# Performance work log

Hardware: AMD Instinct MI355X
Metric: run time of the kernel (lower is better)

## Reference

```python
import jax, jax.numpy as jnp
import numpy as np
from jax import lax

FPLANE = 256
RATIO = 0.5
C_SHIFT = int(FPLANE * RATIO)  # 128
HALF = C_SHIFT // 2            # 64


def setup_inputs() -> dict:
    key = jax.random.key(0)
    k_x, k_wl, k_bl, k_wr, k_br = jax.random.split(key, 5)
    T, C, H, W = 64, FPLANE, 56, 56
    x = jax.random.normal(k_x, (T, C, H, W), dtype=jnp.float32)
    # Conv3d(HALF -> 1, kernel (3,3,3)); original inits to zero, we use small
    # random weights so the gated path is non-trivial for kernel testing.
    scale = 1.0 / np.sqrt(HALF * 27)
    w_l = jax.random.normal(k_wl, (1, HALF, 3, 3, 3), dtype=jnp.float32) * scale
    b_l = jax.random.normal(k_bl, (1,), dtype=jnp.float32) * 0.01
    w_r = jax.random.normal(k_wr, (1, HALF, 3, 3, 3), dtype=jnp.float32) * scale
    b_r = jax.random.normal(k_br, (1,), dtype=jnp.float32) * 0.01
    return {"x": x, "w_l": w_l, "b_l": b_l, "w_r": w_r, "b_r": b_r}


def _cyclic_pad_t(x):
    # x: (1, C, T, H, W) -> pad 1 frame cyclically along T
    return jnp.concatenate([x[:, :, -1:], x, x[:, :, :1]], axis=2)


def _conv3d(x, w, b):
    # temporal padding VALID (input is cyclically pre-padded), spatial SAME
    y = lax.conv_general_dilated(
        x, w, window_strides=(1, 1, 1),
        padding=[(0, 0), (1, 1), (1, 1)],
        dimension_numbers=("NCDHW", "OIDHW", "NCDHW"))
    return y + b[None, :, None, None, None]


def reference(x, w_l, b_l, w_r, b_r):
    # x: (T, C, H, W) -> (1, C, T, H, W)
    x5 = x.transpose(1, 0, 2, 3)[None]
    x_l = x5[:, :HALF]                 # (1, half, T, H, W)
    x_r = x5[:, HALF:C_SHIFT]
    x_keep = x5[:, C_SHIFT:]

    gate_l = jnp.tanh(_conv3d(_cyclic_pad_t(x_l), w_l, b_l))  # (1,1,T,H,W)
    gate_r = jnp.tanh(_conv3d(_cyclic_pad_t(x_r), w_r, b_r))

    y_l = gate_l * x_l
    y_r = gate_r * x_r
    y_l = jnp.roll(y_l, -1, axis=2) + (x_l - y_l)
    y_r = jnp.roll(y_r, 1, axis=2) + (x_r - y_r)

    y_all = jnp.concatenate([y_l, y_r, x_keep], axis=1)  # (1, C, T, H, W)
    return y_all[0].transpose(1, 0, 2, 3)                # (T, C, H, W)
```

## Files before the change

kernel.cpp:

```cpp
#include <hip/hip_runtime.h>
#include <math.h>

#define T_DIM 64
#define C_DIM 256
#define H_DIM 56
#define W_DIM 56
#define HW    (H_DIM * W_DIM)
#define HW4   (HW / 4)
#define CHW   (C_DIM * HW)
#define THW   (T_DIM * HW)

typedef float nt_float4 __attribute__((ext_vector_type(4)));

__device__ __forceinline__ float rfl(float v) {
    return __int_as_float(__builtin_amdgcn_readfirstlane(__float_as_int(v)));
}

__global__ __launch_bounds__(256) void gate_copy_kernel(
    const float* __restrict__ x,
    const float* __restrict__ w_l,
    const float* __restrict__ b_l,
    const float* __restrict__ w_r,
    const float* __restrict__ b_r,
    float* __restrict__ gbuf,
    float* __restrict__ out)
{
    constexpr int NGATE = 256;
    const int p = blockIdx.x;

    if (p >= NGATE) {
        const int qq     = p - NGATE;
        const int tchunk = qq / 392;
        const int bx2    = qq - tchunk * 392;
        const int tid    = 128 * HW4 + bx2 * 256 + (int)threadIdx.x;
        const int t0     = tchunk * 16;

        const nt_float4* xn4 = (const nt_float4*)x;
        nt_float4*       on4 = (nt_float4*)out;
        const size_t ts = C_DIM * HW4;

        #pragma unroll 4
        for (int i = 0; i < 16; ++i) {
            const size_t idx = (size_t)(t0 + i) * ts + tid;
            nt_float4 v = __builtin_nontemporal_load(&xn4[idx]);
            __builtin_nontemporal_store(v, &on4[idx]);
        }
        return;
    }

    __shared__ float4 red[4][7][64];

    const int xcd  = p & 7;
    const int r    = p >> 3;
    const int tl   = r & 7;
    const int side = (r >> 3) & 1;
    const int hh   = (r >> 4) & 1;
    const int t    = xcd * 8 + tl;

    const int waveid = __builtin_amdgcn_readfirstlane((int)(threadIdx.x >> 6));
    const int lane = threadIdx.x & 63;
    const int wg   = lane & 15;
    const int rg   = lane >> 4;
    const bool act = (wg < 14);
    const int w0   = act ? wg * 4 : 52;
    const int r0   = hh * 28 + rg * 7;
    const bool have_l = (wg > 0);
    const bool have_r = (wg < 13);

    const float* wtab = (side ? w_r : w_l) + waveid * 16 * 27;
    const int c0 = side * 64 + waveid * 16;

    const int tm = (t + 63) & 63, tp = (t + 1) & 63;
    const float* tbase[3] = { x + (size_t)tm * CHW,
                              x + (size_t)t  * CHW,
                              x + (size_t)tp * CHW };

    float acc[7][4];
    #pragma unroll
    for (int j = 0; j < 7; ++j)
        #pragma unroll
        for (int k = 0; k < 4; ++k) acc[j][k] = 0.f;

    #pragma unroll 1
    for (int ci = 0; ci < 16; ++ci) {
        float wgt[27];
        #pragma unroll
        for (int k = 0; k < 27; ++k) wgt[k] = rfl(wtab[ci * 27 + k]);

        #pragma unroll
        for (int dt = 0; dt < 3; ++dt) {
            const float* plane = tbase[dt] + (size_t)(c0 + ci) * HW;

            #pragma unroll
            for (int s9 = 0; s9 < 9; ++s9) {
                const int sr = r0 - 1 + s9;
                bool rv = true;
                int  srow = sr;
                if (s9 == 0)      { rv = (sr >= 0);     srow = rv ? sr : 0; }
                else if (s9 == 8) { rv = (sr < H_DIM);  srow = rv ? sr : (H_DIM - 1); }

                const float* row = plane + srow * W_DIM;
                float4 m  = *(const float4*)(row + w0);
                float  fl = __shfl_up(m.w, 1);
                float  fr = __shfl_down(m.x, 1);

                float f0 = have_l ? fl : 0.f;
                float f1 = m.x, f2 = m.y, f3 = m.z, f4v = m.w;
                float f5 = have_r ? fr : 0.f;
                if ((s9 == 0 || s9 == 8) && !rv) {
                    f0 = 0.f; f1 = 0.f; f2 = 0.f; f3 = 0.f; f4v = 0.f; f5 = 0.f;
                }
                float f[6] = { f0, f1, f2, f3, f4v, f5 };

                const int jlo = (s9 >= 2) ? s9 - 2 : 0;
                const int jhi = (s9 <= 6) ? s9 : 6;
                #pragma unroll
                for (int j = jlo; j <= jhi; ++j) {
                    const int dh = s9 - j;
                    const float w0t = wgt[dt * 9 + dh * 3 + 0];
                    const float w1t = wgt[dt * 9 + dh * 3 + 1];
                    const float w2t = wgt[dt * 9 + dh * 3 + 2];
                    #pragma unroll
                    for (int k = 0; k < 4; ++k)
                        acc[j][k] += w0t * f[k] + w1t * f[k + 1] + w2t * f[k + 2];
                }
            }
        }
    }

    #pragma unroll
    for (int j = 0; j < 7; ++j) {
        float4 v; v.x = acc[j][0]; v.y = acc[j][1]; v.z = acc[j][2]; v.w = acc[j][3];
        red[waveid][j][lane] = v;
    }
    __syncthreads();

    if (waveid == 0 && act) {
        const float bias = side ? b_r[0] : b_l[0];
        float* pp = gbuf + (size_t)side * THW
                         + (size_t)t * HW + r0 * W_DIM + w0;
        #pragma unroll
        for (int j = 0; j < 7; ++j) {
            float4 a = red[0][j][lane], b2 = red[1][j][lane];
            float4 c = red[2][j][lane], d  = red[3][j][lane];
            float4 v;
            v.x = tanhf((a.x + b2.x) + (c.x + d.x) + bias);
            v.y = tanhf((a.y + b2.y) + (c.y + d.y) + bias);
            v.z = tanhf((a.z + b2.z) + (c.z + d.z) + bias);
            v.w = tanhf((a.w + b2.w) + (c.w + d.w) + bias);
            *(float4*)(pp + j * W_DIM) = v;
        }
    }
}

__global__ __launch_bounds__(256) void combine_kernel(
    const float* __restrict__ x,
    const float* __restrict__ g,
    float* __restrict__ out)
{
    const int tid = blockIdx.x * 256 + threadIdx.x;
    const int t0  = blockIdx.y * 16;
    const int c   = tid / HW4;
    const int gb  = tid - c * HW4;

    const float4* x4 = (const float4*)x;
    nt_float4*    on4 = (nt_float4*)out;
    const size_t  ts = C_DIM * HW4;
    const size_t  base = tid;

    if (c < 64) {
        const float4* gl4 = (const float4*)g;
        float4 xv = x4[(size_t)t0 * ts + base];
        float4 g0 = gl4[t0 * HW4 + gb];
        #pragma unroll 4
        for (int i = 0; i < 16; ++i) {
            const int t  = t0 + i;
            const int tp = (t + 1) & 63;
            float4 xn = x4[(size_t)tp * ts + base];
            float4 g1 = gl4[tp * HW4 + gb];
            nt_float4 r;
            r.x = xv.x - g0.x * xv.x + g1.x * xn.x;
            r.y = xv.y - g0.y * xv.y + g1.y * xn.y;
            r.z = xv.z - g0.z * xv.z + g1.z * xn.z;
            r.w = xv.w - g0.w * xv.w + g1.w * xn.w;
            __builtin_nontemporal_store(r, &on4[(size_t)t * ts + base]);
            xv = xn; g0 = g1;
        }
    } else {
        const float4* gr4 = (const float4*)(g + THW);
        const int tmi = (t0 + 63) & 63;
        float4 xm = x4[(size_t)tmi * ts + base];
        float4 gm = gr4[tmi * HW4 + gb];
        #pragma unroll 4
        for (int i = 0; i < 16; ++i) {
            const int t = t0 + i;
            float4 xv = x4[(size_t)t * ts + base];
            float4 g0 = gr4[t * HW4 + gb];
            nt_float4 r;
            r.x = xv.x - g0.x * xv.x + gm.x * xm.x;
            r.y = xv.y - g0.y * xv.y + gm.y * xm.y;
            r.z = xv.z - g0.z * xv.z + gm.z * xm.z;
            r.w = xv.w - g0.w * xv.w + gm.w * xm.w;
            __builtin_nontemporal_store(r, &on4[(size_t)t * ts + base]);
            xm = xv; gm = g0;
        }
    }
}

extern "C" void kernel_launch(void* const* d_in, const int* in_sizes, int n_in,
                              void* d_out, int out_size, void* d_ws, size_t ws_size,
                              hipStream_t stream) {
    const float* x   = (const float*)d_in[0];
    const float* w_l = (const float*)d_in[1];
    const float* b_l = (const float*)d_in[2];
    const float* w_r = (const float*)d_in[3];
    const float* b_r = (const float*)d_in[4];
    float* out  = (float*)d_out;
    float* gbuf = (float*)d_ws;

    const int ngate = 256;
    const int ncopy = 392 * 4;
    gate_copy_kernel<<<ngate + ncopy, 256, 0, stream>>>(x, w_l, b_l, w_r, b_r,
                                                        gbuf, out);
    combine_kernel<<<dim3(392, 4), 256, 0, stream>>>(x, gbuf, out);
}
```

Before: 125.9 us.

## Split gate conv channels across 16 waves with tree reduction in LDS

Raises the gate/copy kernel block size from 256 to 1024 threads, so each gate block uses 16 waves, each handling 4 input channels instead of 16. Per-wave partial sums are combined with a log-step tree reduction through shared memory. The copy blocks are resized to match the new block size. The aim is to shorten the serial channel loop and spread the gate work over more waves, at the cost of extra barriers, more reduction traffic, and possible register pressure under 1024-thread launch bounds.

```diff
diff --git a/kernel.cpp b/kernel.cpp
--- a/kernel.cpp
+++ b/kernel.cpp
@@ -16,7 +16,7 @@
     return __int_as_float(__builtin_amdgcn_readfirstlane(__float_as_int(v)));
 }
 
-__global__ __launch_bounds__(256) void gate_copy_kernel(
+__global__ __launch_bounds__(1024) void gate_copy_kernel(
     const float* __restrict__ x,
     const float* __restrict__ w_l,
     const float* __restrict__ b_l,
@@ -26,13 +26,15 @@
     float* __restrict__ out)
 {
     constexpr int NGATE = 256;
+    __shared__ float4 red[8][7][64];
+
     const int p = blockIdx.x;
 
     if (p >= NGATE) {
         const int qq     = p - NGATE;
-        const int tchunk = qq / 392;
-        const int bx2    = qq - tchunk * 392;
-        const int tid    = 128 * HW4 + bx2 * 256 + (int)threadIdx.x;
+        const int tchunk = qq / 98;
+        const int bx2    = qq - tchunk * 98;
+        const int tid    = 128 * HW4 + bx2 * 1024 + (int)threadIdx.x;
         const int t0     = tchunk * 16;
 
         const nt_float4* xn4 = (const nt_float4*)x;
@@ -47,8 +49,6 @@
         }
         return;
     }
-
-    __shared__ float4 red[4][7][64];
 
     const int xcd  = p & 7;
     const int r    = p >> 3;
@@ -67,8 +67,8 @@
     const bool have_l = (wg > 0);
     const bool have_r = (wg < 13);
 
-    const float* wtab = (side ? w_r : w_l) + waveid * 16 * 27;
-    const int c0 = side * 64 + waveid * 16;
+    const float* wtab = (side ? w_r : w_l) + waveid * 4 * 27;
+    const int c0 = side * 64 + waveid * 4;
 
     const int tm = (t + 63) & 63, tp = (t + 1) & 63;
     const float* tbase[3] = { x + (size_t)tm * CHW,
@@ -82,7 +82,7 @@
         for (int k = 0; k < 4; ++k) acc[j][k] = 0.f;
 
     #pragma unroll 1
-    for (int ci = 0; ci < 16; ++ci) {
+    for (int ci = 0; ci < 4; ++ci) {
         float wgt[27];
         #pragma unroll
         for (int k = 0; k < 27; ++k) wgt[k] = rfl(wtab[ci * 27 + k]);
@@ -129,11 +129,26 @@
     }
 
     #pragma unroll
-    for (int j = 0; j < 7; ++j) {
-        float4 v; v.x = acc[j][0]; v.y = acc[j][1]; v.z = acc[j][2]; v.w = acc[j][3];
-        red[waveid][j][lane] = v;
-    }
-    __syncthreads();
+    for (int n = 8; n >= 1; n >>= 1) {
+        if (waveid >= n && waveid < 2 * n) {
+            #pragma unroll
+            for (int j = 0; j < 7; ++j) {
+                float4 v; v.x = acc[j][0]; v.y = acc[j][1];
+                          v.z = acc[j][2]; v.w = acc[j][3];
+                red[waveid - n][j][lane] = v;
+            }
+        }
+        __syncthreads();
+        if (waveid < n) {
+            #pragma unroll
+            for (int j = 0; j < 7; ++j) {
+                float4 v = red[waveid][j][lane];
+                acc[j][0] += v.x; acc[j][1] += v.y;
+                acc[j][2] += v.z; acc[j][3] += v.w;
+            }
+        }
+        if (n > 1) __syncthreads();
+    }
 
     if (waveid == 0 && act) {
         const float bias = side ? b_r[0] : b_l[0];
@@ -141,13 +156,11 @@
                          + (size_t)t * HW + r0 * W_DIM + w0;
         #pragma unroll
         for (int j = 0; j < 7; ++j) {
-            float4 a = red[0][j][lane], b2 = red[1][j][lane];
-            float4 c = red[2][j][lane], d  = red[3][j][lane];
             float4 v;
-            v.x = tanhf((a.x + b2.x) + (c.x + d.x) + bias);
-            v.y = tanhf((a.y + b2.y) + (c.y + d.y) + bias);
-            v.z = tanhf((a.z + b2.z) + (c.z + d.z) + bias);
-            v.w = tanhf((a.w + b2.w) + (c.w + d.w) + bias);
+            v.x = tanhf(acc[j][0] + bias);
+            v.y = tanhf(acc[j][1] + bias);
+            v.z = tanhf(acc[j][2] + bias);
+            v.w = tanhf(acc[j][3] + bias);
             *(float4*)(pp + j * W_DIM) = v;
         }
     }
@@ -219,8 +232,8 @@
     float* gbuf = (float*)d_ws;
 
     const int ngate = 256;
-    const int ncopy = 392 * 4;
-    gate_copy_kernel<<<ngate + ncopy, 256, 0, stream>>>(x, w_l, b_l, w_r, b_r,
-                                                        gbuf, out);
+    const int ncopy = 392;
+    gate_copy_kernel<<<ngate + ncopy, 1024, 0, stream>>>(x, w_l, b_l, w_r, b_r,
+                                                         gbuf, out);
     combine_kernel<<<dim3(392, 4), 256, 0, stream>>>(x, gbuf, out);
 }
```

Result: slower. 289.7 us (+130.1%).

## Split gate conv channel reduction across four blocks with atomic last-block finalize

Applied to the files above, without the earlier changes.

Splits each gate tile's 64-channel reduction into four blocks of 16 channels, raising the gate grid from 256 to 1024 blocks. Each block writes partial sums to a workspace buffer, and an atomic counter picks the last-arriving block to sum the four partials, apply bias and tanh, and write the gate. This targets the long per-block serial conv loop and poor GPU fill from only 256 gate blocks. In exchange it adds partial-sum global traffic, a memset launch, and fence/atomic synchronisation.

```diff
diff --git a/kernel.cpp b/kernel.cpp
--- a/kernel.cpp
+++ b/kernel.cpp
@@ -9,6 +9,10 @@
 #define HW4   (HW / 4)
 #define CHW   (C_DIM * HW)
 #define THW   (T_DIM * HW)
+#define PL4   (THW / 4)
+#define TS4   (C_DIM * HW4)
+#define NGATE 1024
+#define NCOPY 1568
 
 typedef float nt_float4 __attribute__((ext_vector_type(4)));
 
@@ -22,26 +26,27 @@
     const float* __restrict__ b_l,
     const float* __restrict__ w_r,
     const float* __restrict__ b_r,
+    float* __restrict__ pbuf,
     float* __restrict__ gbuf,
-    float* __restrict__ out)
+    float* __restrict__ out,
+    unsigned int* __restrict__ cnt)
 {
-    constexpr int NGATE = 256;
-    const int p = blockIdx.x;
+    const int p   = blockIdx.x;
+    const int tid = threadIdx.x;
 
     if (p >= NGATE) {
         const int qq     = p - NGATE;
         const int tchunk = qq / 392;
         const int bx2    = qq - tchunk * 392;
-        const int tid    = 128 * HW4 + bx2 * 256 + (int)threadIdx.x;
+        const int col    = 128 * HW4 + bx2 * 256 + tid;
         const int t0     = tchunk * 16;
 
         const nt_float4* xn4 = (const nt_float4*)x;
         nt_float4*       on4 = (nt_float4*)out;
-        const size_t ts = C_DIM * HW4;
 
         #pragma unroll 4
         for (int i = 0; i < 16; ++i) {
-            const size_t idx = (size_t)(t0 + i) * ts + tid;
+            const size_t idx = (size_t)(t0 + i) * TS4 + col;
             nt_float4 v = __builtin_nontemporal_load(&xn4[idx]);
             __builtin_nontemporal_store(v, &on4[idx]);
         }
@@ -49,16 +54,19 @@
     }
 
     __shared__ float4 red[4][7][64];
-
-    const int xcd  = p & 7;
-    const int r    = p >> 3;
-    const int tl   = r & 7;
-    const int side = (r >> 3) & 1;
-    const int hh   = (r >> 4) & 1;
-    const int t    = xcd * 8 + tl;
-
-    const int waveid = __builtin_amdgcn_readfirstlane((int)(threadIdx.x >> 6));
-    const int lane = threadIdx.x & 63;
+    __shared__ int    lastflag;
+
+    const int xcd   = p & 7;
+    const int j     = p >> 3;
+    const int gq    = j & 3;
+    const int tileL = j >> 2;
+    const int tl    = tileL & 7;
+    const int side  = (tileL >> 3) & 1;
+    const int hh    = tileL >> 4;
+    const int t     = xcd * 8 + tl;
+
+    const int waveid = __builtin_amdgcn_readfirstlane(tid >> 6);
+    const int lane = tid & 63;
     const int wg   = lane & 15;
     const int rg   = lane >> 4;
     const bool act = (wg < 14);
@@ -67,8 +75,9 @@
     const bool have_l = (wg > 0);
     const bool have_r = (wg < 13);
 
-    const float* wtab = (side ? w_r : w_l) + waveid * 16 * 27;
-    const int c0 = side * 64 + waveid * 16;
+    const int cw = gq * 16 + waveid * 4;
+    const float* wtab = (side ? w_r : w_l) + cw * 27;
+    const int c0 = side * 64 + cw;
 
     const int tm = (t + 63) & 63, tp = (t + 1) & 63;
     const float* tbase[3] = { x + (size_t)tm * CHW,
@@ -77,12 +86,12 @@
 
     float acc[7][4];
     #pragma unroll
-    for (int j = 0; j < 7; ++j)
+    for (int jj = 0; jj < 7; ++jj)
         #pragma unroll
-        for (int k = 0; k < 4; ++k) acc[j][k] = 0.f;
+        for (int k = 0; k < 4; ++k) acc[jj][k] = 0.f;
 
     #pragma unroll 1
-    for (int ci = 0; ci < 16; ++ci) {
+    for (int ci = 0; ci < 4; ++ci) {
         float wgt[27];
         #pragma unroll
         for (int k = 0; k < 27; ++k) wgt[k] = rfl(wtab[ci * 27 + k]);
@@ -115,40 +124,70 @@
                 const int jlo = (s9 >= 2) ? s9 - 2 : 0;
                 const int jhi = (s9 <= 6) ? s9 : 6;
                 #pragma unroll
-                for (int j = jlo; j <= jhi; ++j) {
-                    const int dh = s9 - j;
+                for (int jj = jlo; jj <= jhi; ++jj) {
+                    const int dh = s9 - jj;
                     const float w0t = wgt[dt * 9 + dh * 3 + 0];
                     const float w1t = wgt[dt * 9 + dh * 3 + 1];
                     const float w2t = wgt[dt * 9 + dh * 3 + 2];
                     #pragma unroll
                     for (int k = 0; k < 4; ++k)
-                        acc[j][k] += w0t * f[k] + w1t * f[k + 1] + w2t * f[k + 2];
+                        acc[jj][k] += w0t * f[k] + w1t * f[k + 1] + w2t * f[k + 2];
                 }
             }
         }
     }
 
     #pragma unroll
-    for (int j = 0; j < 7; ++j) {
-        float4 v; v.x = acc[j][0]; v.y = acc[j][1]; v.z = acc[j][2]; v.w = acc[j][3];
-        red[waveid][j][lane] = v;
+    for (int jj = 0; jj < 7; ++jj) {
+        float4 v; v.x = acc[jj][0]; v.y = acc[jj][1];
+                  v.z = acc[jj][2]; v.w = acc[jj][3];
+        red[waveid][jj][lane] = v;
     }
     __syncthreads();
 
-    if (waveid == 0 && act) {
+    const int sg = side * 4 + gq;
+    if (waveid == 0) {
+        if (act) {
+            float* pp = pbuf + (size_t)sg * THW
+                             + (size_t)t * HW + r0 * W_DIM + w0;
+            #pragma unroll
+            for (int jj = 0; jj < 7; ++jj) {
+                float4 a = red[0][jj][lane], b2 = red[1][jj][lane];
+                float4 c = red[2][jj][lane], d  = red[3][jj][lane];
+                float4 v;
+                v.x = (a.x + b2.x) + (c.x + d.x);
+                v.y = (a.y + b2.y) + (c.y + d.y);
+                v.z = (a.z + b2.z) + (c.z + d.z);
+                v.w = (a.w + b2.w) + (c.w + d.w);
+                *(float4*)(pp + jj * W_DIM) = v;
+            }
+        }
+        __threadfence();
+        if (tid == 0) {
+            unsigned old = atomicAdd(&cnt[xcd * 32 + tileL], 1u);
+            lastflag = (old == 3u);
+        }
+    }
+    __syncthreads();
+
+    if (lastflag) {
+        __threadfence();
         const float bias = side ? b_r[0] : b_l[0];
-        float* pp = gbuf + (size_t)side * THW
-                         + (size_t)t * HW + r0 * W_DIM + w0;
-        #pragma unroll
-        for (int j = 0; j < 7; ++j) {
-            float4 a = red[0][j][lane], b2 = red[1][j][lane];
-            float4 c = red[2][j][lane], d  = red[3][j][lane];
+        const float4* p4 = (const float4*)pbuf;
+        float4* g4 = (float4*)gbuf;
+        const int base4 = t * HW4 + hh * 392;
+
+        for (int i = tid; i < 392; i += 256) {
+            float4 a = p4[(size_t)(side * 4 + 0) * PL4 + base4 + i];
+            float4 b = p4[(size_t)(side * 4 + 1) * PL4 + base4 + i];
+            float4 c = p4[(size_t)(side * 4 + 2) * PL4 + base4 + i];
+            float4 d = p4[(size_t)(side * 4 + 3) * PL4 + base4 + i];
             float4 v;
-            v.x = tanhf((a.x + b2.x) + (c.x + d.x) + bias);
-            v.y = tanhf((a.y + b2.y) + (c.y + d.y) + bias);
-            v.z = tanhf((a.z + b2.z) + (c.z + d.z) + bias);
-            v.w = tanhf((a.w + b2.w) + (c.w + d.w) + bias);
-            *(float4*)(pp + j * W_DIM) = v;
+            v.x = tanhf((a.x + b.x) + (c.x + d.x) + bias);
+            v.y = tanhf((a.y + b.y) + (c.y + d.y) + bias);
+            v.z = tanhf((a.z + b.z) + (c.z + d.z) + bias);
+            v.w = tanhf((a.w + b.w) + (c.w + d.w) + bias);
+            g4[(size_t)side * PL4 + base4 + i] = v;
         }
     }
 }
@@ -165,43 +204,42 @@
 
     const float4* x4 = (const float4*)x;
     nt_float4*    on4 = (nt_float4*)out;
-    const size_t  ts = C_DIM * HW4;
     const size_t  base = tid;
 
     if (c < 64) {
         const float4* gl4 = (const float4*)g;
-        float4 xv = x4[(size_t)t0 * ts + base];
+        float4 xv = x4[(size_t)t0 * TS4 + base];
         float4 g0 = gl4[t0 * HW4 + gb];
         #pragma unroll 4
         for (int i = 0; i < 16; ++i) {
             const int t  = t0 + i;
             const int tp = (t + 1) & 63;
-            float4 xn = x4[(size_t)tp * ts + base];
+            float4 xn = x4[(size_t)tp * TS4 + base];
             float4 g1 = gl4[tp * HW4 + gb];
             nt_float4 r;
             r.x = xv.x - g0.x * xv.x + g1.x * xn.x;
             r.y = xv.y - g0.y * xv.y + g1.y * xn.y;
             r.z = xv.z - g0.z * xv.z + g1.z * xn.z;
             r.w = xv.w - g0.w * xv.w + g1.w * xn.w;
-            __builtin_nontemporal_store(r, &on4[(size_t)t * ts + base]);
+            __builtin_nontemporal_store(r, &on4[(size_t)t * TS4 + base]);
             xv = xn; g0 = g1;
         }
     } else {
         const float4* gr4 = (const float4*)(g + THW);
         const int tmi = (t0 + 63) & 63;
-        float4 xm = x4[(size_t)tmi * ts + base];
+        float4 xm = x4[(size_t)tmi * TS4 + base];
         float4 gm = gr4[tmi * HW4 + gb];
         #pragma unroll 4
         for (int i = 0; i < 16; ++i) {
             const int t = t0 + i;
-            float4 xv = x4[(size_t)t * ts + base];
+            float4 xv = x4[(size_t)t * TS4 + base];
             float4 g0 = gr4[t * HW4 + gb];
             nt_float4 r;
             r.x = xv.x - g0.x * xv.x + gm.x * xm.x;
             r.y = xv.y - g0.y * xv.y + gm.y * xm.y;
             r.z = xv.z - g0.z * xv.z + gm.z * xm.z;
             r.w = xv.w - g0.w * xv.w + gm.w * xm.w;
-            __builtin_nontemporal_store(r, &on4[(size_t)t * ts + base]);
+            __builtin_nontemporal_store(r, &on4[(size_t)t * TS4 + base]);
             xm = xv; gm = g0;
         }
     }
@@ -216,11 +254,16 @@
     const float* w_r = (const float*)d_in[3];
     const float* b_r = (const float*)d_in[4];
     float* out  = (float*)d_out;
-    float* gbuf = (float*)d_ws;
-
-    const int ngate = 256;
-    const int ncopy = 392 * 4;
-    gate_copy_kernel<<<ngate + ncopy, 256, 0, stream>>>(x, w_l, b_l, w_r, b_r,
-                                                        gbuf, out);
+    float* ws   = (float*)d_ws;
+
+    float* pbuf = ws;
+    float* gbuf = ws + (size_t)8 * THW;
+    unsigned int* cnt = (unsigned int*)(ws + (size_t)10 * THW);
+
+    hipMemsetAsync(cnt, 0, 256 * sizeof(unsigned int), stream);
+
+    gate_copy_kernel<<<NGATE + NCOPY, 256, 0, stream>>>(
+        x, w_l, b_l, w_r, b_r, pbuf, gbuf, out, cnt);
+
     combine_kernel<<<dim3(392, 4), 256, 0, stream>>>(x, gbuf, out);
 }
```

New measurement: 220.0 us. 74.7% more time.
